# Performance work log

Hardware: AMD Instinct MI355X
Metric: run time of the kernel (lower is better)

Reference implementation:

```python
import jax, jax.numpy as jnp
import numpy as np

B, N, S, C, NS = 2, 20000, 1024, 256, 16
RADIUS, HMIN, HMAX = 0.05, -0.02, 0.04
NA, ND = 12, 4
EPS = 1e-5  # BatchNorm eps


def setup_inputs() -> dict:
    key = jax.random.key(0)
    ks = jax.random.split(key, 40)
    def rn(k, shape, scale=0.05):
        return jax.random.normal(k, shape, jnp.float32) * scale
    inp = {
        "xyz": jax.random.uniform(ks[0], (B, N, 3), jnp.float32),
        "new_xyz": jax.random.uniform(ks[1], (B, S, 3), jnp.float32),
        "view_rot": jax.random.normal(ks[2], (B, S, 3, 3), jnp.float32),
        "features": jax.random.normal(ks[3], (B, C, N), jnp.float32),
    }
    i = 4
    for li, (o, ci) in enumerate([(512, C + 3), (256, 512), (256, 256)], 1):
        inp[f"mlp{li}_w"] = rn(ks[i], (o, ci)); inp[f"mlp{li}_b"] = rn(ks[i + 1], (o,))
        inp[f"mlp{li}_g"] = jnp.ones((o,), jnp.float32) + rn(ks[i + 2], (o,), 0.01)
        inp[f"mlp{li}_be"] = rn(ks[i + 3], (o,)); i += 4
    for name in ("c1", "c2"):
        inp[f"{name}_w"] = rn(ks[i], (256, 256)); inp[f"{name}_b"] = rn(ks[i + 1], (256,))
        inp[f"{name}_g"] = jnp.ones((256,), jnp.float32) + rn(ks[i + 2], (256,), 0.01)
        inp[f"{name}_be"] = rn(ks[i + 3], (256,)); i += 4
    inp["c3_w"] = rn(ks[i], (NA * ND * 2, 256)); inp["c3_b"] = rn(ks[i + 1], (NA * ND * 2,))
    return inp


def _bn(x, g, be):  # eval-mode BatchNorm with running_mean=0, running_var=1
    return x * (g / jnp.sqrt(1.0 + EPS)) + be


def _forward(xyz, new_xyz, view_rot, features,
             mlp1_w, mlp1_b, mlp1_g, mlp1_be,
             mlp2_w, mlp2_b, mlp2_g, mlp2_be,
             mlp3_w, mlp3_b, mlp3_g, mlp3_be,
             c1_w, c1_b, c1_g, c1_be,
             c2_w, c2_b, c2_g, c2_be,
             c3_w, c3_b):
    # ---- cylinder query (CUDA kernel math: r = rot @ (p - c), cylinder axis = x) ----
    # computed per rotation row to keep intermediates at (B,S,N) each
    comp = []
    for i in range(3):
        rw = view_rot[:, :, i, :]  # (B,S,3)
        comp.append(jnp.einsum('bsj,bpj->bsp', rw, xyz) - jnp.sum(rw * new_xyz, -1)[..., None])
    xr, yr, zr = comp  # each (B,S,N)
    mask = (yr * yr + zr * zr < RADIUS * RADIUS) & (xr > HMIN) & (xr < HMAX)
    # first-NS valid indices per seed (ascending), pad with first valid (0 if none)
    vals = jnp.where(mask, jnp.arange(N, dtype=jnp.int32), N)  # (B,S,N)
    neg_top, _ = jax.lax.top_k(-vals, NS)
    idx = -neg_top  # (B,S,NS) ascending
    first = idx[..., :1]
    first = jnp.where(first >= N, 0, first)
    idx = jnp.where(idx >= N, first, idx)
    # ---- group ----
    b_ix = jnp.arange(B)[:, None, None]
    g_xyz = xyz[b_ix, idx]                                  # (B,S,NS,3)
    g_feat = jnp.transpose(features, (0, 2, 1))[b_ix, idx]  # (B,S,NS,C)
    diff = (g_xyz - new_xyz[:, :, None, :]) / RADIUS        # normalize_xyz
    rot_xyz = jnp.einsum('bsnk,bskj->bsnj', diff, view_rot)  # rotate_xyz: diff @ rot
    h = jnp.concatenate([rot_xyz, g_feat], axis=-1)          # (B,S,NS,C+3)
    # ---- SharedMLP (1x1 conv2d + BN + ReLU) ----
    for w, bb, g, be in ((mlp1_w, mlp1_b, mlp1_g, mlp1_be),
                         (mlp2_w, mlp2_b, mlp2_g, mlp2_be),
                         (mlp3_w, mlp3_b, mlp3_g, mlp3_be)):
        h = jax.nn.relu(_bn(jnp.einsum('bsnc,oc->bsno', h, w) + bb, g, be))
    h = h.max(axis=2)  # max-pool over samples -> (B,S,256)
    # ---- pointwise conv1d head ----
    h = jax.nn.relu(_bn(jnp.einsum('bsc,oc->bso', h, c1_w) + c1_b, c1_g, c1_be))
    h = jax.nn.relu(_bn(jnp.einsum('bsc,oc->bso', h, c2_w) + c2_b, c2_g, c2_be))
    out = jnp.einsum('bsc,oc->bso', h, c3_w) + c3_b  # (B,S,NA*ND*2)
    return out


def reference(xyz, new_xyz, view_rot, features,
              mlp1_w, mlp1_b, mlp1_g, mlp1_be,
              mlp2_w, mlp2_b, mlp2_g, mlp2_be,
              mlp3_w, mlp3_b, mlp3_g, mlp3_be,
              c1_w, c1_b, c1_g, c1_be,
              c2_w, c2_b, c2_g, c2_be,
              c3_w, c3_b):
    return _forward(xyz, new_xyz, view_rot, features,
                    mlp1_w, mlp1_b, mlp1_g, mlp1_be,
                    mlp2_w, mlp2_b, mlp2_g, mlp2_be,
                    mlp3_w, mlp3_b, mlp3_g, mlp3_be,
                    c1_w, c1_b, c1_g, c1_be,
                    c2_w, c2_b, c2_g, c2_be,
                    c3_w, c3_b)
```

## Files before the change

kernel.cpp:

```cpp
#include <hip/hip_runtime.h>
#include <hip/hip_bf16.h>
#include <stdint.h>
#include <limits.h>

#define B_   2
#define N_   20000
#define S_   1024
#define C_   256
#define NS_  16
#define NQ   (B_ * S_)
#define M_   (NQ * NS_)
#define K1P  288
#define O1   512
#define O2   256
#define O3   256
#define OUTC 96

#define R2C   ((float)(0.05 * 0.05))
#define HMINC ((float)(-0.02))
#define HMAXC ((float)(0.04))

#define GDIM   16
#define GCELLS (GDIM * GDIM * GDIM)
#define GTOT   (B_ * GCELLS)
#define CAP    256

__device__ __forceinline__ unsigned short f2b(float f) {
    union { float f; unsigned int i; } x; x.f = f;
    unsigned int r = x.i + 0x7FFFu + ((x.i >> 16) & 1u);
    return (unsigned short)(r >> 16);
}
__device__ __forceinline__ float b2f(unsigned short u) {
    union { unsigned int i; float f; } x; x.i = ((unsigned int)u) << 16; return x.f;
}

__global__ __launch_bounds__(256) void prep_w123(const float* __restrict__ m1w,
                                                 const float* __restrict__ m2w,
                                                 const float* __restrict__ m3w,
                                                 unsigned short* __restrict__ w1p,
                                                 unsigned short* __restrict__ w2p,
                                                 unsigned short* __restrict__ w3p) {
    int i = blockIdx.x * 256 + threadIdx.x;
    if (i < O1 * K1P) {
        int o = i / K1P, k = i - o * K1P;
        float v = 0.0f;
        if (k < 256)      v = m1w[o * 259 + 3 + k];
        else if (k < 259) v = m1w[o * 259 + (k - 256)];
        w1p[i] = (k < 259) ? f2b(v) : (unsigned short)0;
    } else if (i < O1 * K1P + O2 * 512) {
        int j = i - O1 * K1P;
        w2p[j] = f2b(m2w[j]);
    } else if (i < O1 * K1P + O2 * 512 + O3 * 256) {
        int j = i - O1 * K1P - O2 * 512;
        w3p[j] = f2b(m3w[j]);
    }
}

__global__ __launch_bounds__(256) void prep_head_w(const float* __restrict__ c1w,
                                                   const float* __restrict__ c2w,
                                                   const float* __restrict__ c3w,
                                                   unsigned short* __restrict__ c1wb,
                                                   unsigned short* __restrict__ c2wb,
                                                   unsigned short* __restrict__ c3wb) {
    int i = blockIdx.x * 256 + threadIdx.x;
    if (i < 65536) {
        c1wb[i] = f2b(c1w[i]);
    } else if (i < 131072) {
        c2wb[i - 65536] = f2b(c2w[i - 65536]);
    } else if (i < 163840) {
        int j = i - 131072;
        int o = j >> 8, k = j & 255;
        c3wb[j] = (o < OUTC) ? f2b(c3w[o * 256 + k]) : (unsigned short)0;
    }
}

__global__ __launch_bounds__(256) void transpose_feat(const float* __restrict__ feat,
                                                      unsigned short* __restrict__ feat_t) {
    __shared__ float tile[32][33];
    int n0 = blockIdx.x * 32, c0 = blockIdx.y * 32, b = blockIdx.z;
    int t = threadIdx.x;
    int nl = t & 31;
#pragma unroll
    for (int i = 0; i < 4; ++i) {
        int cl = (t >> 5) + i * 8;
        tile[cl][nl] = feat[((size_t)(b * C_ + c0 + cl)) * N_ + n0 + nl];
    }
    __syncthreads();
    int nr = t >> 3, c4 = (t & 7) * 4;
    ushort4 v;
    v.x = f2b(tile[c4 + 0][nr]);
    v.y = f2b(tile[c4 + 1][nr]);
    v.z = f2b(tile[c4 + 2][nr]);
    v.w = f2b(tile[c4 + 3][nr]);
    *(ushort4*)(feat_t + ((size_t)(b * N_ + n0 + nr)) * C_ + c0 + c4) = v;
}

__global__ __launch_bounds__(256) void grid_zero(int* __restrict__ c) {
    c[blockIdx.x * 256 + threadIdx.x] = 0;
}

__device__ __forceinline__ int cell_of(float px, float py, float pz, int b) {
    int cx = (int)(px * (float)GDIM); cx = min(GDIM - 1, max(0, cx));
    int cy = (int)(py * (float)GDIM); cy = min(GDIM - 1, max(0, cy));
    int cz = (int)(pz * (float)GDIM); cz = min(GDIM - 1, max(0, cz));
    return b * GCELLS + cz * (GDIM * GDIM) + cy * GDIM + cx;
}

__global__ __launch_bounds__(256) void grid_count(const float* __restrict__ xyz,
                                                  int* __restrict__ counts) {
    int i = blockIdx.x * 256 + threadIdx.x;
    if (i < B_ * N_) {
        int b = i / N_;
        const float* p = xyz + (size_t)i * 3;
        atomicAdd(counts + cell_of(p[0], p[1], p[2], b), 1);
    }
}

__global__ __launch_bounds__(256) void grid_scan(const int* __restrict__ counts,
                                                 int* __restrict__ start,
                                                 int* __restrict__ cursor) {
    __shared__ int part[256];
    int t = threadIdx.x;
    int local[32];
    int s = 0;
#pragma unroll
    for (int i = 0; i < 32; ++i) { local[i] = counts[t * 32 + i]; s += local[i]; }
    part[t] = s;
    __syncthreads();
    if (t == 0) {
        int r = 0;
        for (int i = 0; i < 256; ++i) { int x = part[i]; part[i] = r; r += x; }
    }
    __syncthreads();
    int r = part[t];
#pragma unroll
    for (int i = 0; i < 32; ++i) {
        start[t * 32 + i] = r;
        cursor[t * 32 + i] = r;
        r += local[i];
    }
    if (t == 255) start[GTOT] = r;
}

__global__ __launch_bounds__(256) void grid_scatter(const float* __restrict__ xyz,
                                                    int* __restrict__ cursor,
                                                    float4* __restrict__ sorted) {
    int i = blockIdx.x * 256 + threadIdx.x;
    if (i < B_ * N_) {
        int b = i / N_, n = i - b * N_;
        const float* p = xyz + (size_t)i * 3;
        float px = p[0], py = p[1], pz = p[2];
        int pos = atomicAdd(cursor + cell_of(px, py, pz, b), 1);
        sorted[pos] = make_float4(px, py, pz, __int_as_float(n));
    }
}

__device__ __forceinline__ void sort16(int* buf, int cnt, int lane) {
    asm volatile("s_waitcnt lgkmcnt(0)" ::: "memory");
    __builtin_amdgcn_sched_barrier(0);
    int a0 = INT_MAX, a1 = INT_MAX, a2 = INT_MAX, a3 = INT_MAX;
    if (lane < cnt)       a0 = buf[lane];
    if (lane + 64 < cnt)  a1 = buf[lane + 64];
    if (lane + 128 < cnt) a2 = buf[lane + 128];
    if (lane + 192 < cnt) a3 = buf[lane + 192];
#pragma unroll
    for (int t = 0; t < NS_; ++t) {
        int v = a0, sl = 0;
        if (a1 < v) { v = a1; sl = 1; }
        if (a2 < v) { v = a2; sl = 2; }
        if (a3 < v) { v = a3; sl = 3; }
        int pp = (sl << 6) | lane;
#pragma unroll
        for (int off = 1; off < 64; off <<= 1) {
            int ov = __shfl_xor(v, off);
            int op = __shfl_xor(pp, off);
            if (ov < v) { v = ov; pp = op; }
        }
        if ((pp & 63) == lane) {
            int s = pp >> 6;
            if (s == 0) a0 = INT_MAX;
            else if (s == 1) a1 = INT_MAX;
            else if (s == 2) a2 = INT_MAX;
            else a3 = INT_MAX;
        }
        if (lane == 0) buf[t] = v;
    }
    asm volatile("s_waitcnt lgkmcnt(0)" ::: "memory");
    __builtin_amdgcn_sched_barrier(0);
}

#define SCAN_SPAN(SS, EE)                                                    \
    for (int base = (SS); base < (EE); base += 64) {                         \
        int p = base + lane;                                                 \
        bool m = false; int n = 0;                                           \
        if (p < (EE)) {                                                      \
            float4 v = sorted[p];                                            \
            n = __float_as_int(v.w);                                         \
            float px = v.x, py = v.y, pz = v.z;                              \
            float xr = ((R[0]*px + R[1]*py) + R[2]*pz) - dq0;                \
            float yr = ((R[3]*px + R[4]*py) + R[5]*pz) - dq1;                \
            float zr = ((R[6]*px + R[7]*py) + R[8]*pz) - dq2;                \
            m = ((yr*yr + zr*zr) < R2C) && (xr > HMINC) && (xr < HMAXC);     \
        }                                                                    \
        unsigned long long bal = __ballot(m);                                \
        if (m) {                                                             \
            int pos = cnt + __popcll(bal & ((1ull << lane) - 1ull));         \
            buf[pos] = n;                                                    \
        }                                                                    \
        int h = __popcll(bal);                                               \
        cnt += h; tot += h;                                                  \
        if (cnt > CAP - 64) { sort16(buf, cnt, lane); cnt = NS_; }           \
    }

__global__ __launch_bounds__(256) void cyl_query_grid(const float* __restrict__ new_xyz,
                                                      const float* __restrict__ view_rot,
                                                      const float4* __restrict__ sorted,
                                                      const int* __restrict__ cell_start,
                                                      int* __restrict__ idx_out) {
#pragma clang fp contract(off)
    int w = threadIdx.x >> 6, lane = threadIdx.x & 63;
    int q = blockIdx.x;
    int b = q >> 10;

    __shared__ int bufs[4][CAP];
    __shared__ int tots[4];
    int* buf = bufs[w];

    const float* nq = new_xyz + (size_t)q * 3;
    float qx = nq[0], qy = nq[1], qz = nq[2];
    const float* rp = view_rot + (size_t)q * 9;
    float R[9];
#pragma unroll
    for (int i = 0; i < 9; ++i) R[i] = rp[i];
    float dq0 = (R[0]*qx + R[1]*qy) + R[2]*qz;
    float dq1 = (R[3]*qx + R[4]*qy) + R[5]*qz;
    float dq2 = (R[6]*qx + R[7]*qy) + R[8]*qz;

    int x0 = 0, x1 = GDIM - 1, y0 = 0, y1 = GDIM - 1, z0 = 0, z1 = GDIM - 1;
    bool ok = false;
    {
        float det = R[0]*(R[4]*R[8]-R[5]*R[7])
                  - R[1]*(R[3]*R[8]-R[5]*R[6])
                  + R[2]*(R[3]*R[7]-R[4]*R[6]);
        float adet = fabsf(det);
        if (adet > 1e-30f) {
            ok = true;
            float id = 1.0f / det;
            float m00 = (R[4]*R[8]-R[5]*R[7])*id, m01 = (R[2]*R[7]-R[1]*R[8])*id, m02 = (R[1]*R[5]-R[2]*R[4])*id;
            float m10 = (R[5]*R[6]-R[3]*R[8])*id, m11 = (R[0]*R[8]-R[2]*R[6])*id, m12 = (R[2]*R[3]-R[0]*R[5])*id;
            float m20 = (R[3]*R[7]-R[4]*R[6])*id, m21 = (R[1]*R[6]-R[0]*R[7])*id, m22 = (R[0]*R[4]-R[1]*R[3])*id;
            const float mid = 0.5f * (HMINC + HMAXC);
            const float hh  = 0.5f * (HMAXC - HMINC);
            float cx = qx + m00 * mid, cy = qy + m10 * mid, cz = qz + m20 * mid;
            float ex = hh * fabsf(m00) + 0.05f * sqrtf(m01*m01 + m02*m02);
            float ey = hh * fabsf(m10) + 0.05f * sqrtf(m11*m11 + m12*m12);
            float ez = hh * fabsf(m20) + 0.05f * sqrtf(m21*m21 + m22*m22);
            ex = ex * 1.002f + 1e-3f;
            ey = ey * 1.002f + 1e-3f;
            ez = ez * 1.002f + 1e-3f;
            x0 = (int)fmaxf(0.0f, fminf((float)(GDIM - 1), floorf((cx - ex) * (float)GDIM)));
            x1 = (int)fmaxf(0.0f, fminf((float)(GDIM - 1), floorf((cx + ex) * (float)GDIM)));
            y0 = (int)fmaxf(0.0f, fminf((float)(GDIM - 1), floorf((cy - ey) * (float)GDIM)));
            y1 = (int)fmaxf(0.0f, fminf((float)(GDIM - 1), floorf((cy + ey) * (float)GDIM)));
            z0 = (int)fmaxf(0.0f, fminf((float)(GDIM - 1), floorf((cz - ez) * (float)GDIM)));
            z1 = (int)fmaxf(0.0f, fminf((float)(GDIM - 1), floorf((cz + ez) * (float)GDIM)));
        }
    }

    int nx = x1 - x0 + 1, ny = y1 - y0 + 1, nz = z1 - z0 + 1;
    bool heavy = (!ok) || (ny * nz > 256) || (nx * ny * nz > 512);

    int cnt = 0, tot = 0;
    int cbase = b * GCELLS;

    if (!heavy) {
        int NR = ny * nz;
        int nr_w = (NR - w + 3) >> 2;
        int sl = 0, el = 0;
        if (lane < nr_w) {
            int ri = w + (lane << 2);
            int zi = ri / ny;
            int yi = ri - zi * ny;
            int cid = cbase + (z0 + zi) * (GDIM * GDIM) + (y0 + yi) * GDIM;
            sl = cell_start[cid + x0];
            el = cell_start[cid + x1 + 1];
        }
        for (int j = 0; j < nr_w; ++j) {
            int s = __shfl(sl, j), e = __shfl(el, j);
            SCAN_SPAN(s, e)
        }
    } else {
        int bstart = b * N_;
        int per = (N_ + 3) >> 2;
        int s = bstart + w * per;
        int e = min(bstart + N_, s + per);
        SCAN_SPAN(s, e)
    }

    sort16(buf, cnt, lane);
    if (lane == 0) tots[w] = tot;
    __syncthreads();

    if (w == 0) {
        int cand = bufs[lane >> 4][lane & 15];
        int myv = INT_MAX;
#pragma unroll
        for (int t = 0; t < NS_; ++t) {
            int v = cand, pp = lane;
#pragma unroll
            for (int off = 1; off < 64; off <<= 1) {
                int ov = __shfl_xor(v, off);
                int op = __shfl_xor(pp, off);
                if (ov < v) { v = ov; pp = op; }
            }
            if (lane == t) myv = v;
            if (pp == lane) cand = INT_MAX;
        }
        int tt = tots[0] + tots[1] + tots[2] + tots[3];
        int total = tt < NS_ ? tt : NS_;
        int first = (tt > 0) ? __shfl(myv, 0) : 0;
        if (lane < NS_)
            idx_out[q * NS_ + lane] = (lane < total) ? myv : first;
    }
}

__global__ __launch_bounds__(256) void build_h0(const float* __restrict__ xyz,
                                                const float* __restrict__ new_xyz,
                                                const float* __restrict__ view_rot,
                                                const unsigned short* __restrict__ feat_t,
                                                const int* __restrict__ idxs,
                                                unsigned short* __restrict__ h0) {
#pragma clang fp contract(off)
    int q = blockIdx.x;
    int b = q >> 10;
    int t = threadIdx.x;
    __shared__ int pidx[NS_];
    if (t < NS_) pidx[t] = idxs[q * NS_ + t];
    __syncthreads();

#pragma unroll
    for (int pass = 0; pass < 2; ++pass) {
        int n = pass * 8 + (t >> 5);
        int p = pidx[n];
        uint4 v = *(const uint4*)(feat_t + ((size_t)(b * N_ + p)) * C_ + (t & 31) * 8);
        *(uint4*)(h0 + (size_t)(q * NS_ + n) * K1P + (t & 31) * 8) = v;
    }

    if (t < NS_) {
        int n = t, p = pidx[n];
        const float* pp = xyz + ((size_t)b * N_ + p) * 3;
        const float* nq = new_xyz + (size_t)q * 3;
        float dx = (pp[0] - nq[0]) / 0.05f;
        float dy = (pp[1] - nq[1]) / 0.05f;
        float dz = (pp[2] - nq[2]) / 0.05f;
        const float* rp = view_rot + (size_t)q * 9;
        float r0 = (dx * rp[0] + dy * rp[3]) + dz * rp[6];
        float r1 = (dx * rp[1] + dy * rp[4]) + dz * rp[7];
        float r2 = (dx * rp[2] + dy * rp[5]) + dz * rp[8];
        size_t row = (size_t)(q * NS_ + n) * K1P;
        h0[row + 256] = f2b(r0);
        h0[row + 257] = f2b(r1);
        h0[row + 258] = f2b(r2);
    }
    for (int e = t; e < NS_ * 29; e += 256) {
        int n = e / 29, c = 259 + (e - n * 29);
        h0[(size_t)(q * NS_ + n) * K1P + c] = 0;
    }
}

typedef float f32x4 __attribute__((ext_vector_type(4)));
typedef short s16x8 __attribute__((ext_vector_type(8)));

__global__ __launch_bounds__(256) void gemm_bn_relu(const unsigned short* __restrict__ A,
                                                    const unsigned short* __restrict__ W,
                                                    const float* __restrict__ bias,
                                                    const float* __restrict__ gam,
                                                    const float* __restrict__ bet,
                                                    unsigned short* __restrict__ out,
                                                    int M, int Nn, int K) {
    __shared__ __align__(16) unsigned short As[128 * 32];
    __shared__ __align__(16) unsigned short Bs[128 * 32];
    int tid  = threadIdx.x;
    int lane = tid & 63, wave = tid >> 6;
    int m0 = blockIdx.x * 128, n0 = blockIdx.y * 128;
    int wm = (wave >> 1) * 64, wn = (wave & 1) * 64;

    f32x4 acc[4][4] = {};

    for (int k0 = 0; k0 < K; k0 += 32) {
        __syncthreads();
#pragma unroll
        for (int j = 0; j < 2; ++j) {
            int e = j * 256 + tid;
            int r = e >> 2, c8 = (e & 3) << 3;
            *(uint4*)&As[e * 8] = *(const uint4*)(A + (size_t)(m0 + r) * K + k0 + c8);
            *(uint4*)&Bs[e * 8] = *(const uint4*)(W + (size_t)(n0 + r) * K + k0 + c8);
        }
        __syncthreads();

        int kq = (lane >> 4) * 8, rr = lane & 15;
        s16x8 af[4], bfr[4];
#pragma unroll
        for (int i = 0; i < 4; ++i) af[i]  = *(const s16x8*)&As[(wm + i * 16 + rr) * 32 + kq];
#pragma unroll
        for (int j = 0; j < 4; ++j) bfr[j] = *(const s16x8*)&Bs[(wn + j * 16 + rr) * 32 + kq];
#pragma unroll
        for (int i = 0; i < 4; ++i)
#pragma unroll
            for (int j = 0; j < 4; ++j)
                acc[i][j] = __builtin_amdgcn_mfma_f32_16x16x32_bf16(af[i], bfr[j], acc[i][j], 0, 0, 0);
    }

    float inv = 1.0f / sqrtf(1.0f + 1e-5f);
    int col = lane & 15, rq = (lane >> 4) * 4;
#pragma unroll
    for (int j = 0; j < 4; ++j) {
        int n = n0 + wn + j * 16 + col;
        float sc = gam[n] * inv;
        float tb = bias[n] * sc + bet[n];
#pragma unroll
        for (int i = 0; i < 4; ++i) {
            int mbase = m0 + wm + i * 16 + rq;
#pragma unroll
            for (int r = 0; r < 4; ++r) {
                float v = acc[i][j][r] * sc + tb;
                v = fmaxf(v, 0.0f);
                out[(size_t)(mbase + r) * Nn + n] = f2b(v);
            }
        }
    }
}

__global__ __launch_bounds__(256) void gemm_bn_relu_maxpool(const unsigned short* __restrict__ A,
                                                            const unsigned short* __restrict__ W,
                                                            const float* __restrict__ bias,
                                                            const float* __restrict__ gam,
                                                            const float* __restrict__ bet,
                                                            unsigned short* __restrict__ hp,
                                                            int M, int Nn, int K) {
    __shared__ __align__(16) unsigned short As[128 * 32];
    __shared__ __align__(16) unsigned short Bs[128 * 32];
    int tid  = threadIdx.x;
    int lane = tid & 63, wave = tid >> 6;
    int m0 = blockIdx.x * 128, n0 = blockIdx.y * 128;
    int wm = (wave >> 1) * 64, wn = (wave & 1) * 64;

    f32x4 acc[4][4] = {};

    for (int k0 = 0; k0 < K; k0 += 32) {
        __syncthreads();
#pragma unroll
        for (int j = 0; j < 2; ++j) {
            int e = j * 256 + tid;
            int r = e >> 2, c8 = (e & 3) << 3;
            *(uint4*)&As[e * 8] = *(const uint4*)(A + (size_t)(m0 + r) * K + k0 + c8);
            *(uint4*)&Bs[e * 8] = *(const uint4*)(W + (size_t)(n0 + r) * K + k0 + c8);
        }
        __syncthreads();

        int kq = (lane >> 4) * 8, rr = lane & 15;
        s16x8 af[4], bfr[4];
#pragma unroll
        for (int i = 0; i < 4; ++i) af[i]  = *(const s16x8*)&As[(wm + i * 16 + rr) * 32 + kq];
#pragma unroll
        for (int j = 0; j < 4; ++j) bfr[j] = *(const s16x8*)&Bs[(wn + j * 16 + rr) * 32 + kq];
#pragma unroll
        for (int i = 0; i < 4; ++i)
#pragma unroll
            for (int j = 0; j < 4; ++j)
                acc[i][j] = __builtin_amdgcn_mfma_f32_16x16x32_bf16(af[i], bfr[j], acc[i][j], 0, 0, 0);
    }

    float inv = 1.0f / sqrtf(1.0f + 1e-5f);
    int col = lane & 15;
    int qbase = (m0 + wm) >> 4;
#pragma unroll
    for (int j = 0; j < 4; ++j) {
        int n = n0 + wn + j * 16 + col;
        float sc = gam[n] * inv;
        float tb = bias[n] * sc + bet[n];
#pragma unroll
        for (int i = 0; i < 4; ++i) {
            float mx = 0.0f;
#pragma unroll
            for (int r = 0; r < 4; ++r)
                mx = fmaxf(mx, acc[i][j][r] * sc + tb);
            mx = fmaxf(mx, __shfl_xor(mx, 16, 64));
            mx = fmaxf(mx, __shfl_xor(mx, 32, 64));
            if (lane < 16)
                hp[(size_t)(qbase + i) * Nn + n] = f2b(mx);
        }
    }
}

__global__ __launch_bounds__(256) void gemm_c3(const unsigned short* __restrict__ A,
                                               const unsigned short* __restrict__ W,
                                               const float* __restrict__ bias,
                                               float* __restrict__ out,
                                               int M, int K) {
    __shared__ __align__(16) unsigned short As[128 * 32];
    __shared__ __align__(16) unsigned short Bs[128 * 32];
    int tid  = threadIdx.x;
    int lane = tid & 63, wave = tid >> 6;
    int m0 = blockIdx.x * 128;
    int wm = (wave >> 1) * 64, wn = (wave & 1) * 64;

    f32x4 acc[4][4] = {};

    for (int k0 = 0; k0 < K; k0 += 32) {
        __syncthreads();
#pragma unroll
        for (int j = 0; j < 2; ++j) {
            int e = j * 256 + tid;
            int r = e >> 2, c8 = (e & 3) << 3;
            *(uint4*)&As[e * 8] = *(const uint4*)(A + (size_t)(m0 + r) * K + k0 + c8);
            *(uint4*)&Bs[e * 8] = *(const uint4*)(W + (size_t)r * K + k0 + c8);
        }
        __syncthreads();

        int kq = (lane >> 4) * 8, rr = lane & 15;
        s16x8 af[4], bfr[4];
#pragma unroll
        for (int i = 0; i < 4; ++i) af[i]  = *(const s16x8*)&As[(wm + i * 16 + rr) * 32 + kq];
#pragma unroll
        for (int j = 0; j < 4; ++j) bfr[j] = *(const s16x8*)&Bs[(wn + j * 16 + rr) * 32 + kq];
#pragma unroll
        for (int i = 0; i < 4; ++i)
#pragma unroll
            for (int j = 0; j < 4; ++j)
                acc[i][j] = __builtin_amdgcn_mfma_f32_16x16x32_bf16(af[i], bfr[j], acc[i][j], 0, 0, 0);
    }

    int col = lane & 15, rq = (lane >> 4) * 4;
#pragma unroll
    for (int j = 0; j < 4; ++j) {
        int n = wn + j * 16 + col;
        if (n >= OUTC) continue;
        float bb = bias[n];
#pragma unroll
        for (int i = 0; i < 4; ++i) {
            int mbase = m0 + wm + i * 16 + rq;
#pragma unroll
            for (int r = 0; r < 4; ++r)
                out[(size_t)(mbase + r) * OUTC + n] = acc[i][j][r] + bb;
        }
    }
}

extern "C" void kernel_launch(void* const* d_in, const int* in_sizes, int n_in,
                              void* d_out, int out_size, void* d_ws, size_t ws_size,
                              hipStream_t stream) {
    const float* xyz      = (const float*)d_in[0];
    const float* new_xyz  = (const float*)d_in[1];
    const float* view_rot = (const float*)d_in[2];
    const float* feat     = (const float*)d_in[3];
    const float* m1w = (const float*)d_in[4];
    const float* m1b = (const float*)d_in[5];
    const float* m1g = (const float*)d_in[6];
    const float* m1be= (const float*)d_in[7];
    const float* m2w = (const float*)d_in[8];
    const float* m2b = (const float*)d_in[9];
    const float* m2g = (const float*)d_in[10];
    const float* m2be= (const float*)d_in[11];
    const float* m3w = (const float*)d_in[12];
    const float* m3b = (const float*)d_in[13];
    const float* m3g = (const float*)d_in[14];
    const float* m3be= (const float*)d_in[15];
    const float* c1w = (const float*)d_in[16];
    const float* c1b = (const float*)d_in[17];
    const float* c1g = (const float*)d_in[18];
    const float* c1be= (const float*)d_in[19];
    const float* c2w = (const float*)d_in[20];
    const float* c2b = (const float*)d_in[21];
    const float* c2g = (const float*)d_in[22];
    const float* c2be= (const float*)d_in[23];
    const float* c3w = (const float*)d_in[24];
    const float* c3b = (const float*)d_in[25];

    char* ws = (char*)d_ws;
    int*            idxs = (int*)ws;
    unsigned short* w1p  = (unsigned short*)(ws + 131072);
    unsigned short* w2p  = (unsigned short*)(ws + 425984);
    unsigned short* w3p  = (unsigned short*)(ws + 688128);
    unsigned short* h0   = (unsigned short*)(ws + 819200);
    char*           h1b  = ws + 19693568;
    unsigned short* h1   = (unsigned short*)h1b;
    unsigned short* h2   = h0;
    unsigned short* featt= (unsigned short*)(h1b + 12582912);
    unsigned short* hp   = (unsigned short*)(h1b + 0);
    unsigned short* g1   = (unsigned short*)(h1b + 4194304);
    unsigned short* g2   = (unsigned short*)(h1b + 8388608);
    unsigned short* c1wb = (unsigned short*)(h1b + 12582912);
    unsigned short* c2wb = (unsigned short*)(h1b + 13631488);
    unsigned short* c3wb = (unsigned short*)(h1b + 14680064);
    float4*         srt  = (float4*)(h1b + 0);
    int*            gcnt = (int*)(h1b + 640000);
    int*            gsta = (int*)(h1b + 672768);
    int*            gcur = (int*)(h1b + 705552);

    hipLaunchKernelGGL(prep_w123, dim3((O1 * K1P + O2 * 512 + O3 * 256) / 256), dim3(256), 0, stream,
                       m1w, m2w, m3w, w1p, w2p, w3p);
    hipLaunchKernelGGL(grid_zero, dim3(GTOT / 256), dim3(256), 0, stream, gcnt);
    hipLaunchKernelGGL(grid_count, dim3((B_ * N_ + 255) / 256), dim3(256), 0, stream, xyz, gcnt);
    hipLaunchKernelGGL(grid_scan, dim3(1), dim3(256), 0, stream, gcnt, gsta, gcur);
    hipLaunchKernelGGL(grid_scatter, dim3((B_ * N_ + 255) / 256), dim3(256), 0, stream, xyz, gcur, srt);
    hipLaunchKernelGGL(cyl_query_grid, dim3(NQ), dim3(256), 0, stream,
                       new_xyz, view_rot, srt, gsta, idxs);
    hipLaunchKernelGGL(transpose_feat, dim3(N_ / 32, C_ / 32, B_), dim3(256), 0, stream, feat, featt);
    hipLaunchKernelGGL(build_h0, dim3(NQ), dim3(256), 0, stream, xyz, new_xyz, view_rot, featt, idxs, h0);
    hipLaunchKernelGGL(gemm_bn_relu, dim3(M_ / 128, O1 / 128), dim3(256), 0, stream,
                       h0, w1p, m1b, m1g, m1be, h1, M_, O1, K1P);
    hipLaunchKernelGGL(gemm_bn_relu, dim3(M_ / 128, O2 / 128), dim3(256), 0, stream,
                       h1, w2p, m2b, m2g, m2be, h2, M_, O2, 512);
    hipLaunchKernelGGL(prep_head_w, dim3(163840 / 256), dim3(256), 0, stream,
                       c1w, c2w, c3w, c1wb, c2wb, c3wb);
    hipLaunchKernelGGL(gemm_bn_relu_maxpool, dim3(M_ / 128, O3 / 128), dim3(256), 0, stream,
                       h2, w3p, m3b, m3g, m3be, hp, M_, O3, 256);
    hipLaunchKernelGGL(gemm_bn_relu, dim3(NQ / 128, 256 / 128), dim3(256), 0, stream,
                       hp, c1wb, c1b, c1g, c1be, g1, NQ, 256, 256);
    hipLaunchKernelGGL(gemm_bn_relu, dim3(NQ / 128, 256 / 128), dim3(256), 0, stream,
                       g1, c2wb, c2b, c2g, c2be, g2, NQ, 256, 256);
    hipLaunchKernelGGL(gemm_c3, dim3(NQ / 128), dim3(256), 0, stream,
                       g2, c3wb, c3b, (float*)d_out, NQ, 256);
}
```

Baseline: 286.7 us.

## Fuse MLP2/MLP3+maxpool and head GEMMs, use LDS direct loads, simplify heavy scan

Fuses the second and third shared-MLP GEMMs with the max-pool into one 512-thread kernel that keeps the intermediate 128x256 activation tile in swizzled LDS. This removes the h2 global round trip and a launch. The three head 1x1 convs are fused into one kernel that converts fp32 weights to bf16 on the fly, which drops the separate prep_head_w pass. GEMM operand loads now use global_load_lds direct-to-LDS transfers, and grid zeroing is merged into weight prep. The heavy-seed fallback of the cylinder query now scans raw xyz linearly and stops once NS hits are found. Costs: larger LDS use and lower occupancy in the fused kernels, and repeated per-block weight conversion in the head.

```diff
diff --git a/kernel.cpp b/kernel.cpp
--- a/kernel.cpp
+++ b/kernel.cpp
@@ -30,17 +30,23 @@
     unsigned int r = x.i + 0x7FFFu + ((x.i >> 16) & 1u);
     return (unsigned short)(r >> 16);
 }
-__device__ __forceinline__ float b2f(unsigned short u) {
-    union { unsigned int i; float f; } x; x.i = ((unsigned int)u) << 16; return x.f;
-}
-
-__global__ __launch_bounds__(256) void prep_w123(const float* __restrict__ m1w,
-                                                 const float* __restrict__ m2w,
-                                                 const float* __restrict__ m3w,
-                                                 unsigned short* __restrict__ w1p,
-                                                 unsigned short* __restrict__ w2p,
-                                                 unsigned short* __restrict__ w3p) {
+
+__device__ __forceinline__ void gl16(const unsigned short* g, unsigned short* l) {
+    __builtin_amdgcn_global_load_lds(
+        (const __attribute__((address_space(1))) unsigned int*)g,
+        (__attribute__((address_space(3))) unsigned int*)l,
+        16, 0, 0);
+}
+
+__global__ __launch_bounds__(256) void prep_w123z(const float* __restrict__ m1w,
+                                                  const float* __restrict__ m2w,
+                                                  const float* __restrict__ m3w,
+                                                  unsigned short* __restrict__ w1p,
+                                                  unsigned short* __restrict__ w2p,
+                                                  unsigned short* __restrict__ w3p,
+                                                  int* __restrict__ gcnt) {
     int i = blockIdx.x * 256 + threadIdx.x;
+    if (i < GTOT) gcnt[i] = 0;
     if (i < O1 * K1P) {
         int o = i / K1P, k = i - o * K1P;
         float v = 0.0f;
@@ -56,24 +62,6 @@
     }
 }
 
-__global__ __launch_bounds__(256) void prep_head_w(const float* __restrict__ c1w,
-                                                   const float* __restrict__ c2w,
-                                                   const float* __restrict__ c3w,
-                                                   unsigned short* __restrict__ c1wb,
-                                                   unsigned short* __restrict__ c2wb,
-                                                   unsigned short* __restrict__ c3wb) {
-    int i = blockIdx.x * 256 + threadIdx.x;
-    if (i < 65536) {
-        c1wb[i] = f2b(c1w[i]);
-    } else if (i < 131072) {
-        c2wb[i - 65536] = f2b(c2w[i - 65536]);
-    } else if (i < 163840) {
-        int j = i - 131072;
-        int o = j >> 8, k = j & 255;
-        c3wb[j] = (o < OUTC) ? f2b(c3w[o * 256 + k]) : (unsigned short)0;
-    }
-}
-
 __global__ __launch_bounds__(256) void transpose_feat(const float* __restrict__ feat,
                                                       unsigned short* __restrict__ feat_t) {
     __shared__ float tile[32][33];
@@ -93,10 +81,6 @@
     v.z = f2b(tile[c4 + 2][nr]);
     v.w = f2b(tile[c4 + 3][nr]);
     *(ushort4*)(feat_t + ((size_t)(b * N_ + n0 + nr)) * C_ + c0 + c4) = v;
-}
-
-__global__ __launch_bounds__(256) void grid_zero(int* __restrict__ c) {
-    c[blockIdx.x * 256 + threadIdx.x] = 0;
 }
 
 __device__ __forceinline__ int cell_of(float px, float py, float pz, int b) {
@@ -212,7 +196,8 @@
         if (cnt > CAP - 64) { sort16(buf, cnt, lane); cnt = NS_; }           \
     }
 
-__global__ __launch_bounds__(256) void cyl_query_grid(const float* __restrict__ new_xyz,
+__global__ __launch_bounds__(256) void cyl_query_grid(const float* __restrict__ xyz,
+                                                      const float* __restrict__ new_xyz,
                                                       const float* __restrict__ view_rot,
                                                       const float4* __restrict__ sorted,
                                                       const int* __restrict__ cell_start,
@@ -291,10 +276,28 @@
         }
     } else {
         int bstart = b * N_;
-        int per = (N_ + 3) >> 2;
-        int s = bstart + w * per;
-        int e = min(bstart + N_, s + per);
-        SCAN_SPAN(s, e)
+        int s = bstart + w * (N_ / 4);
+        int e = s + (N_ / 4);
+        for (int base = s; base < e && cnt < NS_; base += 64) {
+            int p = base + lane;
+            bool m = false; int n = 0;
+            if (p < e) {
+                const float* pp = xyz + (size_t)p * 3;
+                n = p - bstart;
+                float px = pp[0], py = pp[1], pz = pp[2];
+                float xr = ((R[0]*px + R[1]*py) + R[2]*pz) - dq0;
+                float yr = ((R[3]*px + R[4]*py) + R[5]*pz) - dq1;
+                float zr = ((R[6]*px + R[7]*py) + R[8]*pz) - dq2;
+                m = ((yr*yr + zr*zr) < R2C) && (xr > HMINC) && (xr < HMAXC);
+            }
+            unsigned long long bal = __ballot(m);
+            if (m) {
+                int pos = cnt + __popcll(bal & ((1ull << lane) - 1ull));
+                buf[pos] = n;
+            }
+            int h = __popcll(bal);
+            cnt += h; tot += h;
+        }
     }
 
     sort16(buf, cnt, lane);
@@ -393,8 +396,8 @@
         for (int j = 0; j < 2; ++j) {
             int e = j * 256 + tid;
             int r = e >> 2, c8 = (e & 3) << 3;
-            *(uint4*)&As[e * 8] = *(const uint4*)(A + (size_t)(m0 + r) * K + k0 + c8);
-            *(uint4*)&Bs[e * 8] = *(const uint4*)(W + (size_t)(n0 + r) * K + k0 + c8);
+            gl16(A + (size_t)(m0 + r) * K + k0 + c8, &As[e * 8]);
+            gl16(W + (size_t)(n0 + r) * K + k0 + c8, &Bs[e * 8]);
         }
         __syncthreads();
 
@@ -431,56 +434,106 @@
     }
 }
 
-__global__ __launch_bounds__(256) void gemm_bn_relu_maxpool(const unsigned short* __restrict__ A,
-                                                            const unsigned short* __restrict__ W,
-                                                            const float* __restrict__ bias,
-                                                            const float* __restrict__ gam,
-                                                            const float* __restrict__ bet,
-                                                            unsigned short* __restrict__ hp,
-                                                            int M, int Nn, int K) {
+__global__ __launch_bounds__(512) void gemm23_pool(const unsigned short* __restrict__ A,
+                                                   const unsigned short* __restrict__ W2,
+                                                   const float* __restrict__ bias2,
+                                                   const float* __restrict__ gam2,
+                                                   const float* __restrict__ bet2,
+                                                   const unsigned short* __restrict__ W3,
+                                                   const float* __restrict__ bias3,
+                                                   const float* __restrict__ gam3,
+                                                   const float* __restrict__ bet3,
+                                                   unsigned short* __restrict__ hp) {
     __shared__ __align__(16) unsigned short As[128 * 32];
-    __shared__ __align__(16) unsigned short Bs[128 * 32];
-    int tid  = threadIdx.x;
-    int lane = tid & 63, wave = tid >> 6;
-    int m0 = blockIdx.x * 128, n0 = blockIdx.y * 128;
-    int wm = (wave >> 1) * 64, wn = (wave & 1) * 64;
-
-    f32x4 acc[4][4] = {};
-
-    for (int k0 = 0; k0 < K; k0 += 32) {
+    __shared__ __align__(16) unsigned short Bs[256 * 32];
+    __shared__ __align__(16) unsigned short H2[128 * 256];
+    int tid = threadIdx.x, lane = tid & 63, wave = tid >> 6;
+    int m0 = blockIdx.x * 128;
+    int wm = (wave >> 1) * 32, wn = (wave & 1) * 128;
+    int kq = (lane >> 4) * 8, rr = lane & 15;
+    int col = lane & 15, rq = (lane >> 4) * 4;
+    float inv = 1.0f / sqrtf(1.0f + 1e-5f);
+
+    f32x4 acc[2][8] = {};
+
+    for (int k0 = 0; k0 < 512; k0 += 32) {
         __syncthreads();
+        {
+            int r = tid >> 2, c8 = (tid & 3) << 3;
+            gl16(A + (size_t)(m0 + r) * 512 + k0 + c8, &As[tid * 8]);
+        }
 #pragma unroll
         for (int j = 0; j < 2; ++j) {
-            int e = j * 256 + tid;
+            int e = j * 512 + tid;
             int r = e >> 2, c8 = (e & 3) << 3;
-            *(uint4*)&As[e * 8] = *(const uint4*)(A + (size_t)(m0 + r) * K + k0 + c8);
-            *(uint4*)&Bs[e * 8] = *(const uint4*)(W + (size_t)(n0 + r) * K + k0 + c8);
+            gl16(W2 + (size_t)r * 512 + k0 + c8, &Bs[e * 8]);
         }
         __syncthreads();
-
-        int kq = (lane >> 4) * 8, rr = lane & 15;
-        s16x8 af[4], bfr[4];
-#pragma unroll
-        for (int i = 0; i < 4; ++i) af[i]  = *(const s16x8*)&As[(wm + i * 16 + rr) * 32 + kq];
-#pragma unroll
-        for (int j = 0; j < 4; ++j) bfr[j] = *(const s16x8*)&Bs[(wn + j * 16 + rr) * 32 + kq];
-#pragma unroll
-        for (int i = 0; i < 4; ++i)
-#pragma unroll
-            for (int j = 0; j < 4; ++j)
-                acc[i][j] = __builtin_amdgcn_mfma_f32_16x16x32_bf16(af[i], bfr[j], acc[i][j], 0, 0, 0);
-    }
-
-    float inv = 1.0f / sqrtf(1.0f + 1e-5f);
-    int col = lane & 15;
+        s16x8 af[2], bf[8];
+#pragma unroll
+        for (int i = 0; i < 2; ++i) af[i] = *(const s16x8*)&As[(wm + i * 16 + rr) * 32 + kq];
+#pragma unroll
+        for (int j = 0; j < 8; ++j) bf[j] = *(const s16x8*)&Bs[(wn + j * 16 + rr) * 32 + kq];
+#pragma unroll
+        for (int i = 0; i < 2; ++i)
+#pragma unroll
+            for (int j = 0; j < 8; ++j)
+                acc[i][j] = __builtin_amdgcn_mfma_f32_16x16x32_bf16(af[i], bf[j], acc[i][j], 0, 0, 0);
+    }
+
+#pragma unroll
+    for (int j = 0; j < 8; ++j) {
+        int n = wn + j * 16 + col;
+        float sc = gam2[n] * inv;
+        float tb = bias2[n] * sc + bet2[n];
+#pragma unroll
+        for (int i = 0; i < 2; ++i) {
+#pragma unroll
+            for (int r = 0; r < 4; ++r) {
+                int row = wm + i * 16 + rq + r;
+                float v = fmaxf(acc[i][j][r] * sc + tb, 0.0f);
+                *(unsigned short*)((char*)H2 + row * 512 + ((2 * n) ^ ((row & 7) << 4))) = f2b(v);
+            }
+        }
+    }
+
+#pragma unroll
+    for (int i = 0; i < 2; ++i)
+#pragma unroll
+        for (int j = 0; j < 8; ++j) acc[i][j] = (f32x4){0.f, 0.f, 0.f, 0.f};
+
+    for (int k0 = 0; k0 < 256; k0 += 32) {
+        __syncthreads();
+#pragma unroll
+        for (int j = 0; j < 2; ++j) {
+            int e = j * 512 + tid;
+            int r = e >> 2, c8 = (e & 3) << 3;
+            gl16(W3 + (size_t)r * 256 + k0 + c8, &Bs[e * 8]);
+        }
+        __syncthreads();
+        s16x8 af[2], bf[8];
+#pragma unroll
+        for (int i = 0; i < 2; ++i) {
+            int row = wm + i * 16 + rr;
+            af[i] = *(const s16x8*)((const char*)H2 + row * 512 + ((2 * (k0 + kq)) ^ ((row & 7) << 4)));
+        }
+#pragma unroll
+        for (int j = 0; j < 8; ++j) bf[j] = *(const s16x8*)&Bs[(wn + j * 16 + rr) * 32 + kq];
+#pragma unroll
+        for (int i = 0; i < 2; ++i)
+#pragma unroll
+            for (int j = 0; j < 8; ++j)
+                acc[i][j] = __builtin_amdgcn_mfma_f32_16x16x32_bf16(af[i], bf[j], acc[i][j], 0, 0, 0);
+    }
+
     int qbase = (m0 + wm) >> 4;
 #pragma unroll
-    for (int j = 0; j < 4; ++j) {
-        int n = n0 + wn + j * 16 + col;
-        float sc = gam[n] * inv;
-        float tb = bias[n] * sc + bet[n];
-#pragma unroll
-        for (int i = 0; i < 4; ++i) {
+    for (int j = 0; j < 8; ++j) {
+        int n = wn + j * 16 + col;
+        float sc = gam3[n] * inv;
+        float tb = bias3[n] * sc + bet3[n];
+#pragma unroll
+        for (int i = 0; i < 2; ++i) {
             float mx = 0.0f;
 #pragma unroll
             for (int r = 0; r < 4; ++r)
@@ -488,61 +541,127 @@
             mx = fmaxf(mx, __shfl_xor(mx, 16, 64));
             mx = fmaxf(mx, __shfl_xor(mx, 32, 64));
             if (lane < 16)
-                hp[(size_t)(qbase + i) * Nn + n] = f2b(mx);
-        }
-    }
-}
-
-__global__ __launch_bounds__(256) void gemm_c3(const unsigned short* __restrict__ A,
-                                               const unsigned short* __restrict__ W,
-                                               const float* __restrict__ bias,
-                                               float* __restrict__ out,
-                                               int M, int K) {
-    __shared__ __align__(16) unsigned short As[128 * 32];
-    __shared__ __align__(16) unsigned short Bs[128 * 32];
-    int tid  = threadIdx.x;
-    int lane = tid & 63, wave = tid >> 6;
-    int m0 = blockIdx.x * 128;
-    int wm = (wave >> 1) * 64, wn = (wave & 1) * 64;
-
-    f32x4 acc[4][4] = {};
-
-    for (int k0 = 0; k0 < K; k0 += 32) {
+                hp[(size_t)(qbase + i) * 256 + n] = f2b(mx);
+        }
+    }
+}
+
+__device__ __forceinline__ void head_gemm(const unsigned short* __restrict__ act,
+                                          unsigned short* __restrict__ Ws,
+                                          const float* __restrict__ Wg, int wrows,
+                                          int tid, int lane, int wn, f32x4 acc[4][4]) {
+    int kq = (lane >> 4) * 8, rr = lane & 15;
+    for (int k0 = 0; k0 < 256; k0 += 32) {
         __syncthreads();
-#pragma unroll
-        for (int j = 0; j < 2; ++j) {
-            int e = j * 256 + tid;
-            int r = e >> 2, c8 = (e & 3) << 3;
-            *(uint4*)&As[e * 8] = *(const uint4*)(A + (size_t)(m0 + r) * K + k0 + c8);
-            *(uint4*)&Bs[e * 8] = *(const uint4*)(W + (size_t)r * K + k0 + c8);
+        if (tid < wrows) {
+            const float* wr = Wg + (size_t)tid * 256 + k0;
+#pragma unroll
+            for (int u = 0; u < 8; ++u) {
+                float4 a = *(const float4*)(wr + 4 * u);
+                ushort4 pk;
+                pk.x = f2b(a.x); pk.y = f2b(a.y); pk.z = f2b(a.z); pk.w = f2b(a.w);
+                *(ushort4*)&Ws[tid * 40 + 4 * u] = pk;
+            }
+        } else {
+            ushort4 z = {0, 0, 0, 0};
+#pragma unroll
+            for (int u = 0; u < 8; ++u) *(ushort4*)&Ws[tid * 40 + 4 * u] = z;
         }
         __syncthreads();
-
-        int kq = (lane >> 4) * 8, rr = lane & 15;
-        s16x8 af[4], bfr[4];
-#pragma unroll
-        for (int i = 0; i < 4; ++i) af[i]  = *(const s16x8*)&As[(wm + i * 16 + rr) * 32 + kq];
-#pragma unroll
-        for (int j = 0; j < 4; ++j) bfr[j] = *(const s16x8*)&Bs[(wn + j * 16 + rr) * 32 + kq];
+        s16x8 af[4], bf[4];
+#pragma unroll
+        for (int i = 0; i < 4; ++i) {
+            int row = i * 16 + rr;
+            af[i] = *(const s16x8*)((const char*)act + row * 512 + ((2 * (k0 + kq)) ^ ((row & 7) << 4)));
+        }
+#pragma unroll
+        for (int j = 0; j < 4; ++j) bf[j] = *(const s16x8*)&Ws[(wn + j * 16 + rr) * 40 + kq];
 #pragma unroll
         for (int i = 0; i < 4; ++i)
 #pragma unroll
             for (int j = 0; j < 4; ++j)
-                acc[i][j] = __builtin_amdgcn_mfma_f32_16x16x32_bf16(af[i], bfr[j], acc[i][j], 0, 0, 0);
-    }
-
-    int col = lane & 15, rq = (lane >> 4) * 4;
+                acc[i][j] = __builtin_amdgcn_mfma_f32_16x16x32_bf16(af[i], bf[j], acc[i][j], 0, 0, 0);
+    }
+}
+
+__global__ __launch_bounds__(256) void head_fused(const unsigned short* __restrict__ hp,
+                                                  const float* __restrict__ c1w, const float* __restrict__ c1b,
+                                                  const float* __restrict__ c1g, const float* __restrict__ c1be,
+                                                  const float* __restrict__ c2w, const float* __restrict__ c2b,
+                                                  const float* __restrict__ c2g, const float* __restrict__ c2be,
+                                                  const float* __restrict__ c3w, const float* __restrict__ c3b,
+                                                  float* __restrict__ out) {
+    __shared__ __align__(16) unsigned short actA[64 * 256];
+    __shared__ __align__(16) unsigned short actB[64 * 256];
+    __shared__ __align__(16) unsigned short Ws[256 * 40];
+    int tid = threadIdx.x, lane = tid & 63, wave = tid >> 6;
+    int q0 = blockIdx.x * 64;
+    int wn = wave * 64, col = lane & 15, rq = (lane >> 4) * 4;
+    float inv = 1.0f / sqrtf(1.0f + 1e-5f);
+
+#pragma unroll
+    for (int j = 0; j < 8; ++j) {
+        int c = j * 256 + tid;
+        int row = c >> 5, cb = c & 31;
+        uint4 v = *(const uint4*)(hp + (size_t)(q0 + row) * 256 + cb * 8);
+        *(uint4*)((char*)actA + row * 512 + (((unsigned)cb << 4) ^ ((row & 7) << 4))) = v;
+    }
+
+    f32x4 acc[4][4];
+
+#pragma unroll
+    for (int i = 0; i < 4; ++i)
+#pragma unroll
+        for (int j = 0; j < 4; ++j) acc[i][j] = (f32x4){0.f, 0.f, 0.f, 0.f};
+    head_gemm(actA, Ws, c1w, 256, tid, lane, wn, acc);
 #pragma unroll
     for (int j = 0; j < 4; ++j) {
         int n = wn + j * 16 + col;
-        if (n >= OUTC) continue;
-        float bb = bias[n];
-#pragma unroll
-        for (int i = 0; i < 4; ++i) {
-            int mbase = m0 + wm + i * 16 + rq;
-#pragma unroll
-            for (int r = 0; r < 4; ++r)
-                out[(size_t)(mbase + r) * OUTC + n] = acc[i][j][r] + bb;
+        float sc = c1g[n] * inv, tb = c1b[n] * sc + c1be[n];
+#pragma unroll
+        for (int i = 0; i < 4; ++i)
+#pragma unroll
+            for (int r = 0; r < 4; ++r) {
+                int row = i * 16 + rq + r;
+                float v = fmaxf(acc[i][j][r] * sc + tb, 0.0f);
+                *(unsigned short*)((char*)actB + row * 512 + ((2 * n) ^ ((row & 7) << 4))) = f2b(v);
+            }
+    }
+
+#pragma unroll
+    for (int i = 0; i < 4; ++i)
+#pragma unroll
+        for (int j = 0; j < 4; ++j) acc[i][j] = (f32x4){0.f, 0.f, 0.f, 0.f};
+    head_gemm(actB, Ws, c2w, 256, tid, lane, wn, acc);
+#pragma unroll
+    for (int j = 0; j < 4; ++j) {
+        int n = wn + j * 16 + col;
+        float sc = c2g[n] * inv, tb = c2b[n] * sc + c2be[n];
+#pragma unroll
+        for (int i = 0; i < 4; ++i)
+#pragma unroll
+            for (int r = 0; r < 4; ++r) {
+                int row = i * 16 + rq + r;
+                float v = fmaxf(acc[i][j][r] * sc + tb, 0.0f);
+                *(unsigned short*)((char*)actA + row * 512 + ((2 * n) ^ ((row & 7) << 4))) = f2b(v);
+            }
+    }
+
+#pragma unroll
+    for (int i = 0; i < 4; ++i)
+#pragma unroll
+        for (int j = 0; j < 4; ++j) acc[i][j] = (f32x4){0.f, 0.f, 0.f, 0.f};
+    head_gemm(actA, Ws, c3w, OUTC, tid, lane, wn, acc);
+#pragma unroll
+    for (int j = 0; j < 4; ++j) {
+        int n = wn + j * 16 + col;
+        if (n < OUTC) {
+            float bb = c3b[n];
+#pragma unroll
+            for (int i = 0; i < 4; ++i)
+#pragma unroll
+                for (int r = 0; r < 4; ++r)
+                    out[(size_t)(q0 + i * 16 + rq + r) * OUTC + n] = acc[i][j][r] + bb;
         }
     }
 }
@@ -583,43 +702,28 @@
     unsigned short* w2p  = (unsigned short*)(ws + 425984);
     unsigned short* w3p  = (unsigned short*)(ws + 688128);
     unsigned short* h0   = (unsigned short*)(ws + 819200);
+    unsigned short* hp   = (unsigned short*)(ws + 819200);
     char*           h1b  = ws + 19693568;
     unsigned short* h1   = (unsigned short*)h1b;
-    unsigned short* h2   = h0;
     unsigned short* featt= (unsigned short*)(h1b + 12582912);
-    unsigned short* hp   = (unsigned short*)(h1b + 0);
-    unsigned short* g1   = (unsigned short*)(h1b + 4194304);
-    unsigned short* g2   = (unsigned short*)(h1b + 8388608);
-    unsigned short* c1wb = (unsigned short*)(h1b + 12582912);
-    unsigned short* c2wb = (unsigned short*)(h1b + 13631488);
-    unsigned short* c3wb = (unsigned short*)(h1b + 14680064);
     float4*         srt  = (float4*)(h1b + 0);
     int*            gcnt = (int*)(h1b + 640000);
     int*            gsta = (int*)(h1b + 672768);
     int*            gcur = (int*)(h1b + 705552);
 
-    hipLaunchKernelGGL(prep_w123, dim3((O1 * K1P + O2 * 512 + O3 * 256) / 256), dim3(256), 0, stream,
-                       m1w, m2w, m3w, w1p, w2p, w3p);
-    hipLaunchKernelGGL(grid_zero, dim3(GTOT / 256), dim3(256), 0, stream, gcnt);
+    hipLaunchKernelGGL(prep_w123z, dim3((O1 * K1P + O2 * 512 + O3 * 256) / 256), dim3(256), 0, stream,
+                       m1w, m2w, m3w, w1p, w2p, w3p, gcnt);
     hipLaunchKernelGGL(grid_count, dim3((B_ * N_ + 255) / 256), dim3(256), 0, stream, xyz, gcnt);
     hipLaunchKernelGGL(grid_scan, dim3(1), dim3(256), 0, stream, gcnt, gsta, gcur);
     hipLaunchKernelGGL(grid_scatter, dim3((B_ * N_ + 255) / 256), dim3(256), 0, stream, xyz, gcur, srt);
     hipLaunchKernelGGL(cyl_query_grid, dim3(NQ), dim3(256), 0, stream,
-                       new_xyz, view_rot, srt, gsta, idxs);
+                       xyz, new_xyz, view_rot, srt, gsta, idxs);
     hipLaunchKernelGGL(transpose_feat, dim3(N_ / 32, C_ / 32, B_), dim3(256), 0, stream, feat, featt);
     hipLaunchKernelGGL(build_h0, dim3(NQ), dim3(256), 0, stream, xyz, new_xyz, view_rot, featt, idxs, h0);
     hipLaunchKernelGGL(gemm_bn_relu, dim3(M_ / 128, O1 / 128), dim3(256), 0, stream,
                        h0, w1p, m1b, m1g, m1be, h1, M_, O1, K1P);
-    hipLaunchKernelGGL(gemm_bn_relu, dim3(M_ / 128, O2 / 128), dim3(256), 0, stream,
-                       h1, w2p, m2b, m2g, m2be, h2, M_, O2, 512);
-    hipLaunchKernelGGL(prep_head_w, dim3(163840 / 256), dim3(256), 0, stream,
-                       c1w, c2w, c3w, c1wb, c2wb, c3wb);
-    hipLaunchKernelGGL(gemm_bn_relu_maxpool, dim3(M_ / 128, O3 / 128), dim3(256), 0, stream,
-                       h2, w3p, m3b, m3g, m3be, hp, M_, O3, 256);
-    hipLaunchKernelGGL(gemm_bn_relu, dim3(NQ / 128, 256 / 128), dim3(256), 0, stream,
-                       hp, c1wb, c1b, c1g, c1be, g1, NQ, 256, 256);
-    hipLaunchKernelGGL(gemm_bn_relu, dim3(NQ / 128, 256 / 128), dim3(256), 0, stream,
-                       g1, c2wb, c2b, c2g, c2be, g2, NQ, 256, 256);
-    hipLaunchKernelGGL(gemm_c3, dim3(NQ / 128), dim3(256), 0, stream,
-                       g2, c3wb, c3b, (float*)d_out, NQ, 256);
-}
+    hipLaunchKernelGGL(gemm23_pool, dim3(M_ / 128), dim3(512), 0, stream,
+                       h1, w2p, m2b, m2g, m2be, w3p, m3b, m3g, m3be, hp);
+    hipLaunchKernelGGL(head_fused, dim3(NQ / 64), dim3(256), 0, stream,
+                       hp, c1w, c1b, c1g, c1be, c2w, c2b, c2g, c2be, c3w, c3b, (float*)d_out);
+}
```

Result: slower. 294.9 us (+2.9%).
